# Optimization experiments

Measured on AMD Instinct MI355X. Metric: run time of the kernel, lower is better.

## Reference

```python
import jax, jax.numpy as jnp
import numpy as np


def setup_inputs() -> dict:
    key = jax.random.key(0)
    k1, k2, k3, k4 = jax.random.split(key, 4)
    vocab, dim, batch, neg_size = 1000000, 128, 16384, 20
    return {
        "target_input": jax.random.randint(k1, (batch,), 0, vocab),
        "context": jax.random.randint(k2, (batch,), 0, vocab),
        "neg": jax.random.randint(k3, (batch, neg_size), 0, vocab),
        "emb": jax.random.normal(k4, (vocab, dim), dtype=jnp.float32),
    }


def reference(target_input, context, neg, emb):
    v = emb[target_input]            # [B, D]
    u = emb[context]                 # [B, D]
    pos = jax.nn.log_sigmoid(jnp.sum(u * v, axis=1))           # [B]
    u_hat = emb[neg]                 # [B, K, D]
    neg_scores = jnp.einsum("bkd,bd->bk", u_hat, v)             # [B, K]
    neg_val = jax.nn.log_sigmoid(-jnp.sum(neg_scores, axis=1))  # [B]
    return -jnp.mean(pos + neg_val)
```

## Files before the change

### kernel.cpp

```cpp
#include <hip/hip_runtime.h>
#include <math.h>

#define DIM 128
#define NEG_K 20

__device__ __forceinline__ float log_sigmoid(float x) {
    float m = fminf(x, 0.0f);
    return m - log1pf(__expf(-fabsf(x)));
}

__global__ __launch_bounds__(256) void sgns_partial_kernel(
    const int* __restrict__ target,
    const int* __restrict__ context,
    const int* __restrict__ neg,
    const float* __restrict__ emb,
    float* __restrict__ partials,
    int B)
{
    const int tid  = blockIdx.x * blockDim.x + threadIdx.x;
    const int lane = threadIdx.x & 63;
    const int sub  = lane & 31;
    const int hw   = tid >> 5;
    const int nHW  = (gridDim.x * blockDim.x) >> 5;

    float local = 0.0f;
    for (int b = hw; b < B; b += nHW) {
        const int tgt = target[b];
        const int ctx = context[b];
        const int4* __restrict__ nbv = (const int4*)(neg + (size_t)b * NEG_K);
        const int4 n0 = nbv[0], n1 = nbv[1], n2 = nbv[2], n3 = nbv[3], n4 = nbv[4];

        const float4 v = *(const float4*)(emb + (size_t)tgt * DIM + sub * 4);
        const float4 u = *(const float4*)(emb + (size_t)ctx * DIM + sub * 4);

        float4 ns = make_float4(0.f, 0.f, 0.f, 0.f);
#define ACC(I) { const float4 un = *(const float4*)(emb + (size_t)(I) * DIM + sub * 4); \
                 ns.x += un.x; ns.y += un.y; ns.z += un.z; ns.w += un.w; }
        ACC(n0.x) ACC(n0.y) ACC(n0.z) ACC(n0.w)
        ACC(n1.x) ACC(n1.y) ACC(n1.z) ACC(n1.w)
        ACC(n2.x) ACC(n2.y) ACC(n2.z) ACC(n2.w)
        ACC(n3.x) ACC(n3.y) ACC(n3.z) ACC(n3.w)
        ACC(n4.x) ACC(n4.y) ACC(n4.z) ACC(n4.w)
#undef ACC

        float pos = u.x * v.x + u.y * v.y + u.z * v.z + u.w * v.w;
        float ng  = ns.x * v.x + ns.y * v.y + ns.z * v.z + ns.w * v.w;

        #pragma unroll
        for (int off = 16; off; off >>= 1) {
            pos += __shfl_xor(pos, off);
            ng  += __shfl_xor(ng,  off);
        }
        if (sub == 0) local += log_sigmoid(pos) + log_sigmoid(-ng);
    }

    #pragma unroll
    for (int off = 32; off; off >>= 1) local += __shfl_xor(local, off);

    __shared__ float wsum[4];
    if (lane == 0) wsum[threadIdx.x >> 6] = local;
    __syncthreads();
    if (threadIdx.x == 0)
        partials[blockIdx.x] = wsum[0] + wsum[1] + wsum[2] + wsum[3];
}

__global__ __launch_bounds__(256) void sgns_reduce_kernel(
    const float* __restrict__ partials, float* __restrict__ out,
    int n, float invB)
{
    float s = 0.0f;
    for (int i = threadIdx.x; i < n; i += 256) s += partials[i];
    #pragma unroll
    for (int off = 32; off; off >>= 1) s += __shfl_xor(s, off);

    __shared__ float wsum[4];
    const int lane = threadIdx.x & 63;
    if (lane == 0) wsum[threadIdx.x >> 6] = s;
    __syncthreads();
    if (threadIdx.x == 0)
        out[0] = -(wsum[0] + wsum[1] + wsum[2] + wsum[3]) * invB;
}

extern "C" void kernel_launch(void* const* d_in, const int* in_sizes, int n_in,
                              void* d_out, int out_size, void* d_ws, size_t ws_size,
                              hipStream_t stream) {
    const int*   target  = (const int*)d_in[0];
    const int*   context = (const int*)d_in[1];
    const int*   neg     = (const int*)d_in[2];
    const float* emb     = (const float*)d_in[3];
    float* out      = (float*)d_out;
    float* partials = (float*)d_ws;
    const int B = in_sizes[0];

    const int threads = 256;
    const int blocks  = (B * 32 + threads - 1) / threads;

    sgns_partial_kernel<<<blocks, threads, 0, stream>>>(target, context, neg,
                                                        emb, partials, B);
    sgns_reduce_kernel<<<1, threads, 0, stream>>>(partials, out, blocks,
                                                  1.0f / (float)B);
}
```

Before: 589.2 us.

## Map one full wavefront per batch row with scalar index loads

Each 64-lane wavefront now processes one batch row, with each lane loading a float2 of every embedding row, where before half-wavefronts did float4 loads. Target, context and negative indices are read via readfirstlane so they become wave-uniform scalar values, which removes the per-lane vector index loads and the int4 negative loads. The grid is resized to one wave per row, and the final per-wave reduction is dropped because only lane 0 accumulates. The trade-off is narrower per-lane loads and twice the number of waves, which could change how the random gathers behave in memory.

```diff
diff --git a/kernel.cpp b/kernel.cpp
--- a/kernel.cpp
+++ b/kernel.cpp
@@ -17,45 +17,42 @@
     float* __restrict__ partials,
     int B)
 {
-    const int tid  = blockIdx.x * blockDim.x + threadIdx.x;
     const int lane = threadIdx.x & 63;
-    const int sub  = lane & 31;
-    const int hw   = tid >> 5;
-    const int nHW  = (gridDim.x * blockDim.x) >> 5;
+    const int wid  = __builtin_amdgcn_readfirstlane(
+                         (blockIdx.x * blockDim.x + threadIdx.x) >> 6);
+    const int nW   = (gridDim.x * blockDim.x) >> 6;
 
     float local = 0.0f;
-    for (int b = hw; b < B; b += nHW) {
-        const int tgt = target[b];
-        const int ctx = context[b];
-        const int4* __restrict__ nbv = (const int4*)(neg + (size_t)b * NEG_K);
-        const int4 n0 = nbv[0], n1 = nbv[1], n2 = nbv[2], n3 = nbv[3], n4 = nbv[4];
+    for (int b = wid; b < B; b += nW) {
+        const int tgt = __builtin_amdgcn_readfirstlane(target[b]);
+        const int ctx = __builtin_amdgcn_readfirstlane(context[b]);
 
-        const float4 v = *(const float4*)(emb + (size_t)tgt * DIM + sub * 4);
-        const float4 u = *(const float4*)(emb + (size_t)ctx * DIM + sub * 4);
+        int ni[NEG_K];
+        const int* __restrict__ nb = neg + (size_t)b * NEG_K;
+        #pragma unroll
+        for (int k = 0; k < NEG_K; ++k)
+            ni[k] = __builtin_amdgcn_readfirstlane(nb[k]);
 
-        float4 ns = make_float4(0.f, 0.f, 0.f, 0.f);
-#define ACC(I) { const float4 un = *(const float4*)(emb + (size_t)(I) * DIM + sub * 4); \
-                 ns.x += un.x; ns.y += un.y; ns.z += un.z; ns.w += un.w; }
-        ACC(n0.x) ACC(n0.y) ACC(n0.z) ACC(n0.w)
-        ACC(n1.x) ACC(n1.y) ACC(n1.z) ACC(n1.w)
-        ACC(n2.x) ACC(n2.y) ACC(n2.z) ACC(n2.w)
-        ACC(n3.x) ACC(n3.y) ACC(n3.z) ACC(n3.w)
-        ACC(n4.x) ACC(n4.y) ACC(n4.z) ACC(n4.w)
-#undef ACC
+        const float2 v = ((const float2*)(emb + (size_t)tgt * DIM))[lane];
+        const float2 u = ((const float2*)(emb + (size_t)ctx * DIM))[lane];
 
-        float pos = u.x * v.x + u.y * v.y + u.z * v.z + u.w * v.w;
-        float ng  = ns.x * v.x + ns.y * v.y + ns.z * v.z + ns.w * v.w;
+        float2 ns = make_float2(0.f, 0.f);
+        #pragma unroll
+        for (int k = 0; k < NEG_K; ++k) {
+            const float2 un = ((const float2*)(emb + (size_t)ni[k] * DIM))[lane];
+            ns.x += un.x; ns.y += un.y;
+        }
+
+        float pos = u.x * v.x + u.y * v.y;
+        float ng  = ns.x * v.x + ns.y * v.y;
 
         #pragma unroll
-        for (int off = 16; off; off >>= 1) {
+        for (int off = 32; off; off >>= 1) {
             pos += __shfl_xor(pos, off);
             ng  += __shfl_xor(ng,  off);
         }
-        if (sub == 0) local += log_sigmoid(pos) + log_sigmoid(-ng);
+        if (lane == 0) local += log_sigmoid(pos) + log_sigmoid(-ng);
     }
-
-    #pragma unroll
-    for (int off = 32; off; off >>= 1) local += __shfl_xor(local, off);
 
     __shared__ float wsum[4];
     if (lane == 0) wsum[threadIdx.x >> 6] = local;
@@ -93,7 +90,7 @@
     const int B = in_sizes[0];
 
     const int threads = 256;
-    const int blocks  = (B * 32 + threads - 1) / threads;
+    const int blocks  = (B + 3) / 4;
 
     sgns_partial_kernel<<<blocks, threads, 0, stream>>>(target, context, neg,
                                                         emb, partials, B);
```

After: 587.0 us. Within noise of the previous version (-0.4%).
